# Kernel tuning notes

Hardware: AMD Instinct MI355X
Metric: run time of the kernel (lower is better)

## Reference

```python
import jax, jax.numpy as jnp
import numpy as np

D = 768
H = 12
HD = D // H  # 64
EPS = 1e-12


def setup_inputs() -> dict:
    key = jax.random.key(0)
    ks = jax.random.split(key, 9)
    B, S = 4, 2048
    s = 1.0 / np.sqrt(D)
    inp = {
        "hidden_states": jax.random.normal(ks[0], (B, S, D), dtype=jnp.float32),
        "Wq": jax.random.normal(ks[1], (D, D), dtype=jnp.float32) * s,
        "bq": jnp.zeros((D,), dtype=jnp.float32),
        "Wk": jax.random.normal(ks[2], (D, D), dtype=jnp.float32) * s,
        "bk": jnp.zeros((D,), dtype=jnp.float32),
        "Wv": jax.random.normal(ks[3], (D, D), dtype=jnp.float32) * s,
        "bv": jnp.zeros((D,), dtype=jnp.float32),
        "Wo": jax.random.normal(ks[4], (D, D), dtype=jnp.float32) * s,
        "bo": jnp.zeros((D,), dtype=jnp.float32),
    }
    return inp


def _heads(x):
    # [B,S,D] -> [B,H,S,HD]
    B, S, _ = x.shape
    return x.reshape(B, S, H, HD).transpose(0, 2, 1, 3)


def reference(hidden_states, Wq, bq, Wk, bk, Wv, bv, Wo, bo):
    q = _heads(hidden_states @ Wq.T + bq)
    k = _heads(hidden_states @ Wk.T + bk)
    v = _heads(hidden_states @ Wv.T + bv)
    # NOTE: original code does NOT scale by 1/sqrt(head_dim)
    scores = jnp.einsum("bhqd,bhkd->bhqk", q, k)
    probs = jax.nn.softmax(scores, axis=-1)
    ctx = jnp.einsum("bhqk,bhkd->bhqd", probs, v)
    B, _, S, _ = ctx.shape
    ctx = ctx.transpose(0, 2, 1, 3).reshape(B, S, D)
    # output dense + residual
    h = ctx @ Wo.T + bo + hidden_states
    # custom LayerNorm: unbiased std, divide by (std + eps), no affine applied
    mean = jnp.mean(h, axis=-1, keepdims=True)
    std = jnp.sqrt(jnp.var(h, axis=-1, keepdims=True, ddof=1))
    return (h - mean) / (std + EPS)
```

## Files before the change

kernel.cpp:

```cpp
#include <hip/hip_runtime.h>

typedef unsigned short u16;
typedef unsigned int   u32;
typedef __attribute__((ext_vector_type(4))) u32    u32x4;
typedef __attribute__((ext_vector_type(4))) u16    u16x4;
typedef __attribute__((ext_vector_type(8))) u16    u16x8;
typedef __attribute__((ext_vector_type(8))) __bf16 bf16x8;
typedef __attribute__((ext_vector_type(4))) float  f32x4;

#define LOG2E 1.4426950408889634f

__device__ __forceinline__ u16 f2bf(float f) {
    u32 u = __builtin_bit_cast(u32, f);
    return (u16)((u + 0x7FFFu + ((u >> 16) & 1u)) >> 16);
}
__device__ __forceinline__ u32 pk2(float a, float b) {
#if __has_builtin(__builtin_amdgcn_cvt_pk_bf16_f32)
    return __builtin_bit_cast(u32, __builtin_amdgcn_cvt_pk_bf16_f32(a, b));
#else
    return (u32)f2bf(a) | ((u32)f2bf(b) << 16);
#endif
}
__device__ __forceinline__ u16x4 pack4(f32x4 v) {
    u32 lo = pk2(v[0], v[1]), hi = pk2(v[2], v[3]);
    u32 both[2] = {lo, hi};
    return __builtin_bit_cast(u16x4, *(unsigned long long*)both);
}
__device__ __forceinline__ float fexp2(float x) {
#if __has_builtin(__builtin_amdgcn_exp2f)
    return __builtin_amdgcn_exp2f(x);
#else
    float r;
    asm("v_exp_f32 %0, %1" : "=v"(r) : "v"(x));
    return r;
#endif
}
__device__ __forceinline__ bf16x8 ldfrag(const u16* p) {
    return __builtin_bit_cast(bf16x8, *(const u32x4*)p);
}

__global__ __launch_bounds__(256) void convert(
    const float* __restrict__ X,
    const float* __restrict__ Wq, const float* __restrict__ Wk,
    const float* __restrict__ Wv, const float* __restrict__ Wo,
    u16* __restrict__ Xb, u16* __restrict__ Wqb, u16* __restrict__ Wkb,
    u16* __restrict__ Wvb, u16* __restrict__ Wob)
{
    const int NX = 1572864;
    const int NW = 147456;
    int i = blockIdx.x * 256 + threadIdx.x;
    const float* src; u16* dst; int off; float sc = 1.0f;
    if (i < NX)               { src = X;  dst = Xb;  off = i; }
    else if (i < NX + NW)     { src = Wq; dst = Wqb; off = i - NX; sc = LOG2E; }
    else if (i < NX + 2 * NW) { src = Wk; dst = Wkb; off = i - NX - NW; }
    else if (i < NX + 3 * NW) { src = Wv; dst = Wvb; off = i - NX - 2 * NW; }
    else                      { src = Wo; dst = Wob; off = i - NX - 3 * NW; }
    f32x4 v = *(const f32x4*)&src[(size_t)off * 4];
    f32x4 s4 = {sc, sc, sc, sc};
    v *= s4;
    *(u16x4*)&dst[(size_t)off * 4] = pack4(v);
}

__global__ __launch_bounds__(256) void gemm_qkv(
    const u16* __restrict__ Xb,
    const u16* __restrict__ Wqb, const u16* __restrict__ Wkb, const u16* __restrict__ Wvb,
    const float* __restrict__ bq, const float* __restrict__ bk, const float* __restrict__ bv,
    u16* __restrict__ Qo, u16* __restrict__ Ko, u16* __restrict__ Vt)
{
    const int which = blockIdx.z;
    const u16* W      = (which == 0) ? Wqb : ((which == 1) ? Wkb : Wvb);
    const float* bias = (which == 0) ? bq : ((which == 1) ? bk : bv);
    const float scale = (which == 0) ? LOG2E : 1.0f;

    __shared__ __align__(16) u16 sA[128 * 40];
    __shared__ __align__(16) u16 sB[128 * 40];

    const int tid  = threadIdx.x;
    const int wave = tid >> 6, lane = tid & 63;
    const int quad = lane >> 4, l16 = lane & 15;
    const int wr = wave >> 1, wc = wave & 1;
    const int m0 = blockIdx.x * 128, n0 = blockIdx.y * 128;

    const int r0 = tid >> 2,            c0 = (tid & 3) * 8;
    const int r1 = (256 + tid) >> 2,    c1 = ((256 + tid) & 3) * 8;

    f32x4 acc[4][4] = {};
    u32x4 ra0, ra1, rb0, rb1;

    ra0 = *(const u32x4*)&Xb[(size_t)(m0 + r0) * 768 + c0];
    ra1 = *(const u32x4*)&Xb[(size_t)(m0 + r1) * 768 + c1];
    rb0 = *(const u32x4*)&W [(size_t)(n0 + r0) * 768 + c0];
    rb1 = *(const u32x4*)&W [(size_t)(n0 + r1) * 768 + c1];

    for (int k0 = 0; k0 < 768; k0 += 32) {
        __syncthreads();
        *(u32x4*)&sA[r0 * 40 + c0] = ra0;
        *(u32x4*)&sA[r1 * 40 + c1] = ra1;
        *(u32x4*)&sB[r0 * 40 + c0] = rb0;
        *(u32x4*)&sB[r1 * 40 + c1] = rb1;
        int kn = (k0 + 32) % 768;
        ra0 = *(const u32x4*)&Xb[(size_t)(m0 + r0) * 768 + kn + c0];
        ra1 = *(const u32x4*)&Xb[(size_t)(m0 + r1) * 768 + kn + c1];
        rb0 = *(const u32x4*)&W [(size_t)(n0 + r0) * 768 + kn + c0];
        rb1 = *(const u32x4*)&W [(size_t)(n0 + r1) * 768 + kn + c1];
        __syncthreads();

        bf16x8 af[4], bfr[4];
#pragma unroll
        for (int i = 0; i < 4; ++i)
            af[i] = ldfrag(&sA[(wr * 64 + i * 16 + l16) * 40 + quad * 8]);
#pragma unroll
        for (int j = 0; j < 4; ++j)
            bfr[j] = ldfrag(&sB[(wc * 64 + j * 16 + l16) * 40 + quad * 8]);
#pragma unroll
        for (int i = 0; i < 4; ++i)
#pragma unroll
            for (int j = 0; j < 4; ++j)
                acc[i][j] = __builtin_amdgcn_mfma_f32_16x16x32_bf16(af[i], bfr[j], acc[i][j], 0, 0, 0);
    }

    if (which < 2) {
        u16* out = (which == 0) ? Qo : Ko;
#pragma unroll
        for (int j = 0; j < 4; ++j) {
            int n = n0 + wc * 64 + j * 16 + l16;
            float bvv = bias[n] * scale;
            int h = n >> 6, hd = n & 63;
#pragma unroll
            for (int i = 0; i < 4; ++i) {
#pragma unroll
                for (int r = 0; r < 4; ++r) {
                    int m = m0 + wr * 64 + i * 16 + quad * 4 + r;
                    int b = m >> 11, s = m & 2047;
                    out[(((size_t)(b * 12 + h) * 2048) + s) * 64 + hd] =
                        f2bf(acc[i][j][r] + bvv);
                }
            }
        }
    } else {
#pragma unroll
        for (int j = 0; j < 4; ++j) {
            int n = n0 + wc * 64 + j * 16 + l16;
            float bvv = bias[n];
            int h = n >> 6, hd = n & 63;
            f32x4 b4 = {bvv, bvv, bvv, bvv};
#pragma unroll
            for (int i = 0; i < 4; ++i) {
                int m = m0 + wr * 64 + i * 16 + quad * 4;
                int b = m >> 11, s = m & 2047;
                *(u16x4*)&Vt[((size_t)(b * 12 + h) * 64 + hd) * 2048 + s] = pack4(acc[i][j] + b4);
            }
        }
    }
}

__global__ __launch_bounds__(256, 3) void attn(
    const u16* __restrict__ Q, const u16* __restrict__ K, const u16* __restrict__ Vt,
    u16* __restrict__ ctx)
{
    const int bid = blockIdx.x;
    const int xcd = bid & 7, slot = bid >> 3;
    const int bh = xcd * 6 + (slot % 6);
    const int q0 = (slot / 6) * 128;
    const int b = bh / 12, h = bh % 12;
    const u16* Qb  = Q  + (size_t)bh * (2048 * 64);
    const u16* Kb  = K  + (size_t)bh * (2048 * 64);
    const u16* Vtb = Vt + (size_t)bh * (64 * 2048);

    __shared__ __align__(16) u16 sK [64 * 72];
    __shared__ __align__(16) u16 sVt[64 * 72];
    __shared__ __align__(16) u16 sPt[128 * 72];

    const int tid = threadIdx.x;
    const int wave = tid >> 6, lane = tid & 63;
    const int quad = lane >> 4, l16 = lane & 15;

    const int kr0 = tid >> 3,           kc0 = (tid & 7) * 8;
    const int kr1 = (256 + tid) >> 3,   kc1 = ((256 + tid) & 7) * 8;

    bf16x8 qf[2][2];
#pragma unroll
    for (int jn = 0; jn < 2; ++jn)
#pragma unroll
        for (int ks = 0; ks < 2; ++ks)
            qf[jn][ks] = ldfrag(&Qb[(size_t)(q0 + wave * 32 + jn * 16 + l16) * 64 + ks * 32 + quad * 8]);

    bf16x8 vones;
    {
        u16x8 o;
#pragma unroll
        for (int t = 0; t < 8; ++t) o[t] = 0x3F80;
        vones = __builtin_bit_cast(bf16x8, o);
    }

    f32x4 oacc[2][4] = {};
    f32x4 Lacc[2] = {};

    u32x4 rk0, rk1, rv0, rv1;
    rk0 = *(const u32x4*)&Kb [(size_t)kr0 * 64 + kc0];
    rk1 = *(const u32x4*)&Kb [(size_t)kr1 * 64 + kc1];
    rv0 = *(const u32x4*)&Vtb[(size_t)kr0 * 2048 + kc0];
    rv1 = *(const u32x4*)&Vtb[(size_t)kr1 * 2048 + kc1];

    for (int kt = 0; kt < 2048; kt += 64) {
        __syncthreads();
        *(u32x4*)&sK [kr0 * 72 + kc0] = rk0;
        *(u32x4*)&sK [kr1 * 72 + kc1] = rk1;
        *(u32x4*)&sVt[kr0 * 72 + kc0] = rv0;
        *(u32x4*)&sVt[kr1 * 72 + kc1] = rv1;
        int ktn = (kt + 64) & 2047;
        rk0 = *(const u32x4*)&Kb [(size_t)(ktn + kr0) * 64 + kc0];
        rk1 = *(const u32x4*)&Kb [(size_t)(ktn + kr1) * 64 + kc1];
        rv0 = *(const u32x4*)&Vtb[(size_t)kr0 * 2048 + ktn + kc0];
        rv1 = *(const u32x4*)&Vtb[(size_t)kr1 * 2048 + ktn + kc1];
        __syncthreads();

        f32x4 sacc[4][2] = {};
#pragma unroll
        for (int ks = 0; ks < 2; ++ks) {
            bf16x8 kf[4];
#pragma unroll
            for (int i = 0; i < 4; ++i)
                kf[i] = ldfrag(&sK[(i * 16 + l16) * 72 + ks * 32 + quad * 8]);
#pragma unroll
            for (int i = 0; i < 4; ++i)
#pragma unroll
                for (int jn = 0; jn < 2; ++jn)
                    sacc[i][jn] = __builtin_amdgcn_mfma_f32_16x16x32_bf16(kf[i], qf[jn][ks], sacc[i][jn], 0, 0, 0);
        }

#pragma unroll
        for (int i = 0; i < 4; ++i) {
#pragma unroll
            for (int jn = 0; jn < 2; ++jn) {
                f32x4 pe;
#pragma unroll
                for (int r = 0; r < 4; ++r) pe[r] = fexp2(sacc[i][jn][r]);
                *(u16x4*)&sPt[(wave * 32 + jn * 16 + l16) * 72 + i * 16 + quad * 4] = pack4(pe);
            }
        }

#pragma unroll
        for (int ks2 = 0; ks2 < 2; ++ks2) {
            bf16x8 pf[2], vf[4];
#pragma unroll
            for (int jn = 0; jn < 2; ++jn)
                pf[jn] = ldfrag(&sPt[(wave * 32 + jn * 16 + l16) * 72 + ks2 * 32 + quad * 8]);
#pragma unroll
            for (int jh = 0; jh < 4; ++jh)
                vf[jh] = ldfrag(&sVt[(jh * 16 + l16) * 72 + ks2 * 32 + quad * 8]);
#pragma unroll
            for (int jn = 0; jn < 2; ++jn) {
#pragma unroll
                for (int jh = 0; jh < 4; ++jh)
                    oacc[jn][jh] = __builtin_amdgcn_mfma_f32_16x16x32_bf16(pf[jn], vf[jh], oacc[jn][jh], 0, 0, 0);
                Lacc[jn] = __builtin_amdgcn_mfma_f32_16x16x32_bf16(pf[jn], vones, Lacc[jn], 0, 0, 0);
            }
        }
    }

#pragma unroll
    for (int jn = 0; jn < 2; ++jn) {
#pragma unroll
        for (int r = 0; r < 4; ++r) {
            float linv = 1.0f / Lacc[jn][r];
            int srow = q0 + wave * 32 + jn * 16 + quad * 4 + r;
            size_t rowbase = ((size_t)(b * 2048 + srow)) * 768 + h * 64;
#pragma unroll
            for (int jh = 0; jh < 4; ++jh)
                ctx[rowbase + jh * 16 + l16] = f2bf(oacc[jn][jh][r] * linv);
        }
    }
}

__global__ __launch_bounds__(256) void gemm_out(
    const u16* __restrict__ A,
    const u16* __restrict__ Wob,
    const float* __restrict__ bo,
    const float* __restrict__ X,
    float* __restrict__ Hout)
{
    __shared__ __align__(16) u16 sA[128 * 40];
    __shared__ __align__(16) u16 sB[128 * 40];

    const int tid = threadIdx.x;
    const int wave = tid >> 6, lane = tid & 63;
    const int quad = lane >> 4, l16 = lane & 15;
    const int wr = wave >> 1, wc = wave & 1;
    const int m0 = blockIdx.x * 128, n0 = blockIdx.y * 128;

    const int r0 = tid >> 2,            c0 = (tid & 3) * 8;
    const int r1 = (256 + tid) >> 2,    c1 = ((256 + tid) & 3) * 8;

    f32x4 acc[4][4] = {};
    u32x4 ra0, ra1, rb0, rb1;
    ra0 = *(const u32x4*)&A  [(size_t)(m0 + r0) * 768 + c0];
    ra1 = *(const u32x4*)&A  [(size_t)(m0 + r1) * 768 + c1];
    rb0 = *(const u32x4*)&Wob[(size_t)(n0 + r0) * 768 + c0];
    rb1 = *(const u32x4*)&Wob[(size_t)(n0 + r1) * 768 + c1];

    for (int k0 = 0; k0 < 768; k0 += 32) {
        __syncthreads();
        *(u32x4*)&sA[r0 * 40 + c0] = ra0;
        *(u32x4*)&sA[r1 * 40 + c1] = ra1;
        *(u32x4*)&sB[r0 * 40 + c0] = rb0;
        *(u32x4*)&sB[r1 * 40 + c1] = rb1;
        int kn = (k0 + 32) % 768;
        ra0 = *(const u32x4*)&A  [(size_t)(m0 + r0) * 768 + kn + c0];
        ra1 = *(const u32x4*)&A  [(size_t)(m0 + r1) * 768 + kn + c1];
        rb0 = *(const u32x4*)&Wob[(size_t)(n0 + r0) * 768 + kn + c0];
        rb1 = *(const u32x4*)&Wob[(size_t)(n0 + r1) * 768 + kn + c1];
        __syncthreads();

        bf16x8 af[4], bfr[4];
#pragma unroll
        for (int i = 0; i < 4; ++i)
            af[i] = ldfrag(&sA[(wr * 64 + i * 16 + l16) * 40 + quad * 8]);
#pragma unroll
        for (int j = 0; j < 4; ++j)
            bfr[j] = ldfrag(&sB[(wc * 64 + j * 16 + l16) * 40 + quad * 8]);
#pragma unroll
        for (int i = 0; i < 4; ++i)
#pragma unroll
            for (int j = 0; j < 4; ++j)
                acc[i][j] = __builtin_amdgcn_mfma_f32_16x16x32_bf16(af[i], bfr[j], acc[i][j], 0, 0, 0);
    }

#pragma unroll
    for (int j = 0; j < 4; ++j) {
        int n = n0 + wc * 64 + j * 16 + l16;
        float bv_ = bo[n];
#pragma unroll
        for (int i = 0; i < 4; ++i) {
#pragma unroll
            for (int r = 0; r < 4; ++r) {
                size_t m = m0 + wr * 64 + i * 16 + quad * 4 + r;
                Hout[m * 768 + n] = acc[i][j][r] + bv_ + X[m * 768 + n];
            }
        }
    }
}

__global__ __launch_bounds__(256) void lnorm(const float* __restrict__ Hs, float* __restrict__ out)
{
    const int row = blockIdx.x;
    const float* hr = Hs + (size_t)row * 768;
    const int tid = threadIdx.x;
    float v0 = hr[tid], v1 = hr[tid + 256], v2 = hr[tid + 512];
    float s = v0 + v1 + v2;
    float ss = v0 * v0 + v1 * v1 + v2 * v2;
#pragma unroll
    for (int off = 1; off < 64; off <<= 1) {
        s  += __shfl_xor(s, off);
        ss += __shfl_xor(ss, off);
    }
    __shared__ float red[8];
    const int wave = tid >> 6, lane = tid & 63;
    if (lane == 0) { red[wave] = s; red[4 + wave] = ss; }
    __syncthreads();
    s  = red[0] + red[1] + red[2] + red[3];
    ss = red[4] + red[5] + red[6] + red[7];
    float mean = s * (1.0f / 768.0f);
    float var = fmaxf((ss - 768.0f * mean * mean) * (1.0f / 767.0f), 0.0f);
    float inv = 1.0f / (sqrtf(var) + 1e-12f);
    float* orow = out + (size_t)row * 768;
    orow[tid]       = (v0 - mean) * inv;
    orow[tid + 256] = (v1 - mean) * inv;
    orow[tid + 512] = (v2 - mean) * inv;
}

extern "C" void kernel_launch(void* const* d_in, const int* in_sizes, int n_in,
                              void* d_out, int out_size, void* d_ws, size_t ws_size,
                              hipStream_t stream)
{
    const float* X  = (const float*)d_in[0];
    const float* Wq = (const float*)d_in[1];
    const float* bq = (const float*)d_in[2];
    const float* Wk = (const float*)d_in[3];
    const float* bk = (const float*)d_in[4];
    const float* Wv = (const float*)d_in[5];
    const float* bv = (const float*)d_in[6];
    const float* Wo = (const float*)d_in[7];
    const float* bo = (const float*)d_in[8];
    float* out = (float*)d_out;

    const size_t TE = (size_t)8192 * 768;
    const size_t WN = (size_t)768 * 768;
    u16* ws  = (u16*)d_ws;
    u16* Xb  = ws;
    u16* Qw  = ws + TE;
    u16* Kw  = ws + 2 * TE;
    u16* Vt  = ws + 3 * TE;
    u16* Wqb = ws + 4 * TE;
    u16* Wkb = Wqb + WN;
    u16* Wvb = Wqb + 2 * WN;
    u16* Wob = Wqb + 3 * WN;
    u16* Cw  = Xb;
    float* Hw = (float*)(ws + TE);

    convert<<<8448, 256, 0, stream>>>(X, Wq, Wk, Wv, Wo, Xb, Wqb, Wkb, Wvb, Wob);
    gemm_qkv<<<dim3(64, 6, 3), 256, 0, stream>>>(Xb, Wqb, Wkb, Wvb, bq, bk, bv, Qw, Kw, Vt);
    attn<<<768, 256, 0, stream>>>(Qw, Kw, Vt, Cw);
    gemm_out<<<dim3(64, 6), 256, 0, stream>>>(Cw, Wob, bo, X, Hw);
    lnorm<<<8192, 256, 0, stream>>>(Hw, out);
}
```

Baseline: 268.1 us.

## Deepen GEMM K-tiles to 64, fuse QKV weights, store pre-LN residual in bf16

Both projection GEMMs now stage 64-wide K slices per iteration, which halves the number of barrier pairs and global-load rounds. The QKV GEMM uses one concatenated weight buffer, relying on Wq/Wk/Wv being contiguous, and indexes a 2D grid instead of branching on blockIdx.z. The output GEMM writes the residual sum in bf16 instead of fp32, which halves the intermediate traffic into layernorm but loses precision in the normalized output.

```diff
diff --git a/kernel.cpp b/kernel.cpp
--- a/kernel.cpp
+++ b/kernel.cpp
@@ -10,6 +10,10 @@
 
 #define LOG2E 1.4426950408889634f
 
+__device__ __forceinline__ float bf2f(u16 x) {
+    u32 u = ((u32)x) << 16;
+    return __builtin_bit_cast(float, u);
+}
 __device__ __forceinline__ u16 f2bf(float f) {
     u32 u = __builtin_bit_cast(u32, f);
     return (u16)((u + 0x7FFFu + ((u >> 16) & 1u)) >> 16);
@@ -62,68 +66,74 @@
 }
 
 __global__ __launch_bounds__(256) void gemm_qkv(
-    const u16* __restrict__ Xb,
-    const u16* __restrict__ Wqb, const u16* __restrict__ Wkb, const u16* __restrict__ Wvb,
+    const u16* __restrict__ Xb, const u16* __restrict__ Wcat,
     const float* __restrict__ bq, const float* __restrict__ bk, const float* __restrict__ bv,
     u16* __restrict__ Qo, u16* __restrict__ Ko, u16* __restrict__ Vt)
 {
-    const int which = blockIdx.z;
-    const u16* W      = (which == 0) ? Wqb : ((which == 1) ? Wkb : Wvb);
-    const float* bias = (which == 0) ? bq : ((which == 1) ? bk : bv);
-    const float scale = (which == 0) ? LOG2E : 1.0f;
-
-    __shared__ __align__(16) u16 sA[128 * 40];
-    __shared__ __align__(16) u16 sB[128 * 40];
+    __shared__ __align__(16) u16 sA[128 * 72];
+    __shared__ __align__(16) u16 sB[128 * 72];
 
     const int tid  = threadIdx.x;
     const int wave = tid >> 6, lane = tid & 63;
     const int quad = lane >> 4, l16 = lane & 15;
     const int wr = wave >> 1, wc = wave & 1;
-    const int m0 = blockIdx.x * 128, n0 = blockIdx.y * 128;
-
-    const int r0 = tid >> 2,            c0 = (tid & 3) * 8;
-    const int r1 = (256 + tid) >> 2,    c1 = ((256 + tid) & 3) * 8;
+    const int m0 = blockIdx.x * 128;
+    const int ny = blockIdx.y;
+    const int which = ny / 6;
+    const int n0 = ny * 128;
+    const int n_in = (ny % 6) * 128;
+
+    int rr[4], cc[4];
+#pragma unroll
+    for (int p = 0; p < 4; ++p) { int c = p * 256 + tid; rr[p] = c >> 3; cc[p] = (c & 7) * 8; }
 
     f32x4 acc[4][4] = {};
-    u32x4 ra0, ra1, rb0, rb1;
-
-    ra0 = *(const u32x4*)&Xb[(size_t)(m0 + r0) * 768 + c0];
-    ra1 = *(const u32x4*)&Xb[(size_t)(m0 + r1) * 768 + c1];
-    rb0 = *(const u32x4*)&W [(size_t)(n0 + r0) * 768 + c0];
-    rb1 = *(const u32x4*)&W [(size_t)(n0 + r1) * 768 + c1];
-
-    for (int k0 = 0; k0 < 768; k0 += 32) {
-        __syncthreads();
-        *(u32x4*)&sA[r0 * 40 + c0] = ra0;
-        *(u32x4*)&sA[r1 * 40 + c1] = ra1;
-        *(u32x4*)&sB[r0 * 40 + c0] = rb0;
-        *(u32x4*)&sB[r1 * 40 + c1] = rb1;
-        int kn = (k0 + 32) % 768;
-        ra0 = *(const u32x4*)&Xb[(size_t)(m0 + r0) * 768 + kn + c0];
-        ra1 = *(const u32x4*)&Xb[(size_t)(m0 + r1) * 768 + kn + c1];
-        rb0 = *(const u32x4*)&W [(size_t)(n0 + r0) * 768 + kn + c0];
-        rb1 = *(const u32x4*)&W [(size_t)(n0 + r1) * 768 + kn + c1];
-        __syncthreads();
-
-        bf16x8 af[4], bfr[4];
-#pragma unroll
-        for (int i = 0; i < 4; ++i)
-            af[i] = ldfrag(&sA[(wr * 64 + i * 16 + l16) * 40 + quad * 8]);
-#pragma unroll
-        for (int j = 0; j < 4; ++j)
-            bfr[j] = ldfrag(&sB[(wc * 64 + j * 16 + l16) * 40 + quad * 8]);
-#pragma unroll
-        for (int i = 0; i < 4; ++i)
+    u32x4 ra[4], rb[4];
+#pragma unroll
+    for (int p = 0; p < 4; ++p) {
+        ra[p] = *(const u32x4*)&Xb  [(size_t)(m0 + rr[p]) * 768 + cc[p]];
+        rb[p] = *(const u32x4*)&Wcat[(size_t)(n0 + rr[p]) * 768 + cc[p]];
+    }
+
+    for (int k0 = 0; k0 < 768; k0 += 64) {
+        __syncthreads();
+#pragma unroll
+        for (int p = 0; p < 4; ++p) {
+            *(u32x4*)&sA[rr[p] * 72 + cc[p]] = ra[p];
+            *(u32x4*)&sB[rr[p] * 72 + cc[p]] = rb[p];
+        }
+        int kn = k0 + 64; if (kn == 768) kn = 0;
+#pragma unroll
+        for (int p = 0; p < 4; ++p) {
+            ra[p] = *(const u32x4*)&Xb  [(size_t)(m0 + rr[p]) * 768 + kn + cc[p]];
+            rb[p] = *(const u32x4*)&Wcat[(size_t)(n0 + rr[p]) * 768 + kn + cc[p]];
+        }
+        __syncthreads();
+
+#pragma unroll
+        for (int ks = 0; ks < 2; ++ks) {
+            bf16x8 af[4], bfr[4];
+#pragma unroll
+            for (int i = 0; i < 4; ++i)
+                af[i] = ldfrag(&sA[(wr * 64 + i * 16 + l16) * 72 + ks * 32 + quad * 8]);
 #pragma unroll
             for (int j = 0; j < 4; ++j)
-                acc[i][j] = __builtin_amdgcn_mfma_f32_16x16x32_bf16(af[i], bfr[j], acc[i][j], 0, 0, 0);
-    }
-
+                bfr[j] = ldfrag(&sB[(wc * 64 + j * 16 + l16) * 72 + ks * 32 + quad * 8]);
+#pragma unroll
+            for (int i = 0; i < 4; ++i)
+#pragma unroll
+                for (int j = 0; j < 4; ++j)
+                    acc[i][j] = __builtin_amdgcn_mfma_f32_16x16x32_bf16(af[i], bfr[j], acc[i][j], 0, 0, 0);
+        }
+    }
+
+    const float* bias = (which == 0) ? bq : ((which == 1) ? bk : bv);
     if (which < 2) {
         u16* out = (which == 0) ? Qo : Ko;
+        const float scale = (which == 0) ? LOG2E : 1.0f;
 #pragma unroll
         for (int j = 0; j < 4; ++j) {
-            int n = n0 + wc * 64 + j * 16 + l16;
+            int n = n_in + wc * 64 + j * 16 + l16;
             float bvv = bias[n] * scale;
             int h = n >> 6, hd = n & 63;
 #pragma unroll
@@ -140,7 +150,7 @@
     } else {
 #pragma unroll
         for (int j = 0; j < 4; ++j) {
-            int n = n0 + wc * 64 + j * 16 + l16;
+            int n = n_in + wc * 64 + j * 16 + l16;
             float bvv = bias[n];
             int h = n >> 6, hd = n & 63;
             f32x4 b4 = {bvv, bvv, bvv, bvv};
@@ -278,10 +288,10 @@
     const u16* __restrict__ Wob,
     const float* __restrict__ bo,
     const float* __restrict__ X,
-    float* __restrict__ Hout)
-{
-    __shared__ __align__(16) u16 sA[128 * 40];
-    __shared__ __align__(16) u16 sB[128 * 40];
+    u16* __restrict__ Hout)
+{
+    __shared__ __align__(16) u16 sA[128 * 72];
+    __shared__ __align__(16) u16 sB[128 * 72];
 
     const int tid = threadIdx.x;
     const int wave = tid >> 6, lane = tid & 63;
@@ -289,41 +299,48 @@
     const int wr = wave >> 1, wc = wave & 1;
     const int m0 = blockIdx.x * 128, n0 = blockIdx.y * 128;
 
-    const int r0 = tid >> 2,            c0 = (tid & 3) * 8;
-    const int r1 = (256 + tid) >> 2,    c1 = ((256 + tid) & 3) * 8;
+    int rr[4], cc[4];
+#pragma unroll
+    for (int p = 0; p < 4; ++p) { int c = p * 256 + tid; rr[p] = c >> 3; cc[p] = (c & 7) * 8; }
 
     f32x4 acc[4][4] = {};
-    u32x4 ra0, ra1, rb0, rb1;
-    ra0 = *(const u32x4*)&A  [(size_t)(m0 + r0) * 768 + c0];
-    ra1 = *(const u32x4*)&A  [(size_t)(m0 + r1) * 768 + c1];
-    rb0 = *(const u32x4*)&Wob[(size_t)(n0 + r0) * 768 + c0];
-    rb1 = *(const u32x4*)&Wob[(size_t)(n0 + r1) * 768 + c1];
-
-    for (int k0 = 0; k0 < 768; k0 += 32) {
-        __syncthreads();
-        *(u32x4*)&sA[r0 * 40 + c0] = ra0;
-        *(u32x4*)&sA[r1 * 40 + c1] = ra1;
-        *(u32x4*)&sB[r0 * 40 + c0] = rb0;
-        *(u32x4*)&sB[r1 * 40 + c1] = rb1;
-        int kn = (k0 + 32) % 768;
-        ra0 = *(const u32x4*)&A  [(size_t)(m0 + r0) * 768 + kn + c0];
-        ra1 = *(const u32x4*)&A  [(size_t)(m0 + r1) * 768 + kn + c1];
-        rb0 = *(const u32x4*)&Wob[(size_t)(n0 + r0) * 768 + kn + c0];
-        rb1 = *(const u32x4*)&Wob[(size_t)(n0 + r1) * 768 + kn + c1];
-        __syncthreads();
-
-        bf16x8 af[4], bfr[4];
-#pragma unroll
-        for (int i = 0; i < 4; ++i)
-            af[i] = ldfrag(&sA[(wr * 64 + i * 16 + l16) * 40 + quad * 8]);
-#pragma unroll
-        for (int j = 0; j < 4; ++j)
-            bfr[j] = ldfrag(&sB[(wc * 64 + j * 16 + l16) * 40 + quad * 8]);
-#pragma unroll
-        for (int i = 0; i < 4; ++i)
+    u32x4 ra[4], rb[4];
+#pragma unroll
+    for (int p = 0; p < 4; ++p) {
+        ra[p] = *(const u32x4*)&A  [(size_t)(m0 + rr[p]) * 768 + cc[p]];
+        rb[p] = *(const u32x4*)&Wob[(size_t)(n0 + rr[p]) * 768 + cc[p]];
+    }
+
+    for (int k0 = 0; k0 < 768; k0 += 64) {
+        __syncthreads();
+#pragma unroll
+        for (int p = 0; p < 4; ++p) {
+            *(u32x4*)&sA[rr[p] * 72 + cc[p]] = ra[p];
+            *(u32x4*)&sB[rr[p] * 72 + cc[p]] = rb[p];
+        }
+        int kn = k0 + 64; if (kn == 768) kn = 0;
+#pragma unroll
+        for (int p = 0; p < 4; ++p) {
+            ra[p] = *(const u32x4*)&A  [(size_t)(m0 + rr[p]) * 768 + kn + cc[p]];
+            rb[p] = *(const u32x4*)&Wob[(size_t)(n0 + rr[p]) * 768 + kn + cc[p]];
+        }
+        __syncthreads();
+
+#pragma unroll
+        for (int ks = 0; ks < 2; ++ks) {
+            bf16x8 af[4], bfr[4];
+#pragma unroll
+            for (int i = 0; i < 4; ++i)
+                af[i] = ldfrag(&sA[(wr * 64 + i * 16 + l16) * 72 + ks * 32 + quad * 8]);
 #pragma unroll
             for (int j = 0; j < 4; ++j)
-                acc[i][j] = __builtin_amdgcn_mfma_f32_16x16x32_bf16(af[i], bfr[j], acc[i][j], 0, 0, 0);
+                bfr[j] = ldfrag(&sB[(wc * 64 + j * 16 + l16) * 72 + ks * 32 + quad * 8]);
+#pragma unroll
+            for (int i = 0; i < 4; ++i)
+#pragma unroll
+                for (int j = 0; j < 4; ++j)
+                    acc[i][j] = __builtin_amdgcn_mfma_f32_16x16x32_bf16(af[i], bfr[j], acc[i][j], 0, 0, 0);
+        }
     }
 
 #pragma unroll
@@ -335,18 +352,18 @@
 #pragma unroll
             for (int r = 0; r < 4; ++r) {
                 size_t m = m0 + wr * 64 + i * 16 + quad * 4 + r;
-                Hout[m * 768 + n] = acc[i][j][r] + bv_ + X[m * 768 + n];
+                Hout[m * 768 + n] = f2bf(acc[i][j][r] + bv_ + X[m * 768 + n]);
             }
         }
     }
 }
 
-__global__ __launch_bounds__(256) void lnorm(const float* __restrict__ Hs, float* __restrict__ out)
+__global__ __launch_bounds__(256) void lnorm(const u16* __restrict__ Hs, float* __restrict__ out)
 {
     const int row = blockIdx.x;
-    const float* hr = Hs + (size_t)row * 768;
+    const u16* hr = Hs + (size_t)row * 768;
     const int tid = threadIdx.x;
-    float v0 = hr[tid], v1 = hr[tid + 256], v2 = hr[tid + 512];
+    float v0 = bf2f(hr[tid]), v1 = bf2f(hr[tid + 256]), v2 = bf2f(hr[tid + 512]);
     float s = v0 + v1 + v2;
     float ss = v0 * v0 + v1 * v1 + v2 * v2;
 #pragma unroll
@@ -396,10 +413,10 @@
     u16* Wvb = Wqb + 2 * WN;
     u16* Wob = Wqb + 3 * WN;
     u16* Cw  = Xb;
-    float* Hw = (float*)(ws + TE);
+    u16* Hw  = Qw;
 
     convert<<<8448, 256, 0, stream>>>(X, Wq, Wk, Wv, Wo, Xb, Wqb, Wkb, Wvb, Wob);
-    gemm_qkv<<<dim3(64, 6, 3), 256, 0, stream>>>(Xb, Wqb, Wkb, Wvb, bq, bk, bv, Qw, Kw, Vt);
+    gemm_qkv<<<dim3(64, 18), 256, 0, stream>>>(Xb, Wqb, bq, bk, bv, Qw, Kw, Vt);
     attn<<<768, 256, 0, stream>>>(Qw, Kw, Vt, Cw);
     gemm_out<<<dim3(64, 6), 256, 0, stream>>>(Cw, Wob, bo, X, Hw);
     lnorm<<<8192, 256, 0, stream>>>(Hw, out);
```

After: 238.3 us. -11.1%, faster.
